# Performance work log

Hardware: AMD Instinct MI355X
Metric: run time of the kernel (lower is better)

Reference implementation:

```python
import jax, jax.numpy as jnp
import numpy as np
import math

CHANNELS = 512
OUT_CHANNELS = 512
N_HEADS = 8
WINDOW = 4
K_CH = CHANNELS // N_HEADS


def _conv1x1(x, W, b):
    # x: (B, C_in, T), W: (C_out, C_in), b: (C_out,)
    return jnp.einsum('oc,bct->bot', W, x) + b[None, :, None]


def _get_relative_embeddings(emb, length, window=WINDOW):
    # emb: (H, 2*window+1, k_ch) -> (H, 2*length-1, k_ch)
    pad_length = max(length - (window + 1), 0)
    start = max(window + 1 - length, 0)
    e = jnp.pad(emb, ((0, 0), (pad_length, pad_length), (0, 0))) if pad_length > 0 else emb
    return e[:, start:start + 2 * length - 1]


def _relative_to_absolute(x):
    # x: (B, H, L, 2L-1) -> (B, H, L, L)
    b, h, L, _ = x.shape
    x = jnp.pad(x, ((0, 0), (0, 0), (0, 0), (0, 1)))          # (B,H,L,2L)
    xf = x.reshape(b, h, L * 2 * L)
    xf = jnp.pad(xf, ((0, 0), (0, 0), (L - 1, 0)))
    return xf.reshape(b, h, L + 1, 2 * L - 1)[:, :, :L, L - 1:]


def _absolute_to_relative(x):
    # x: (B, H, L, L) -> (B, H, L, 2L-1)
    b, h, L, _ = x.shape
    x = jnp.pad(x, ((0, 0), (0, 0), (0, 0), (0, L - 1)))       # (B,H,L,2L-1)
    xf = x.reshape(b, h, L * (2 * L - 1))
    xf = jnp.pad(xf, ((0, 0), (0, 0), (L, 0)))
    return xf.reshape(b, h, L, 2 * L)[:, :, :, 1:]


def setup_inputs() -> dict:
    key = jax.random.key(0)
    ks = jax.random.split(key, 16)
    B, C, T = 4, CHANNELS, 1024
    xavier = math.sqrt(2.0 / (C + C))
    rel_std = K_CH ** -0.5
    return {
        'x_q': jax.random.normal(ks[0], (B, C, T), jnp.float32),
        'x_k': jax.random.normal(ks[1], (B, C, T), jnp.float32),
        'x_v': jax.random.normal(ks[2], (B, C, T), jnp.float32),
        'Wq': jax.random.normal(ks[3], (C, C), jnp.float32) * xavier,
        'bq': jnp.zeros((C,), jnp.float32),
        'Wk': jax.random.normal(ks[4], (C, C), jnp.float32) * xavier,
        'bk': jnp.zeros((C,), jnp.float32),
        'Wv': jax.random.normal(ks[5], (C, C), jnp.float32) * xavier,
        'bv': jnp.zeros((C,), jnp.float32),
        'Wo': jax.random.normal(ks[6], (OUT_CHANNELS, C), jnp.float32) * xavier,
        'bo': jnp.zeros((OUT_CHANNELS,), jnp.float32),
        'emb_rel_k': jax.random.normal(ks[7], (N_HEADS, 2 * WINDOW + 1, K_CH), jnp.float32) * rel_std,
        'emb_rel_v': jax.random.normal(ks[8], (N_HEADS, 2 * WINDOW + 1, K_CH), jnp.float32) * rel_std,
    }


def reference(x_q, x_k, x_v, Wq, bq, Wk, bk, Wv, bv, Wo, bo, emb_rel_k, emb_rel_v):
    q = _conv1x1(x_q, Wq, bq)
    k = _conv1x1(x_k, Wk, bk)
    v = _conv1x1(x_v, Wv, bv)
    B, C, T = q.shape
    # (B, C, T) -> (B, H, T, k_ch); head h owns contiguous k_ch channel chunk
    qh = q.reshape(B, N_HEADS, K_CH, T).transpose(0, 1, 3, 2) / math.sqrt(K_CH)
    kh = k.reshape(B, N_HEADS, K_CH, T).transpose(0, 1, 3, 2)
    vh = v.reshape(B, N_HEADS, K_CH, T).transpose(0, 1, 3, 2)
    scores = jnp.einsum('bhtd,bhsd->bhts', qh, kh)              # (B,H,T,T)
    rel_k = _get_relative_embeddings(emb_rel_k, T)              # (H,2T-1,d)
    rel_logits = jnp.einsum('bhtd,hmd->bhtm', qh, rel_k)        # (B,H,T,2T-1)
    scores = scores + _relative_to_absolute(rel_logits)
    attn = jax.nn.softmax(scores, axis=-1)
    ctx = jnp.einsum('bhts,bhsd->bhtd', attn, vh)
    rel_w = _absolute_to_relative(attn)                         # (B,H,T,2T-1)
    rel_v = _get_relative_embeddings(emb_rel_v, T)
    ctx = ctx + jnp.einsum('bhtm,hmd->bhtd', rel_w, rel_v)
    out = ctx.transpose(0, 1, 3, 2).reshape(B, C, T)
    return _conv1x1(out, Wo, bo)
```

## Files before the change

### kernel.cpp

```cpp
#include <hip/hip_runtime.h>

#define T_LEN 1024
#define NH 8
#define DH 64
#define CCH 512
#define LOG2E 1.44269504088896340736f

typedef _Float16 f16;
typedef _Float16 f16x8 __attribute__((ext_vector_type(8)));
typedef _Float16 f16x4 __attribute__((ext_vector_type(4)));
typedef float f32x4 __attribute__((ext_vector_type(4)));

__device__ __forceinline__ void dma16(const void* g, void* l)
{
    __builtin_amdgcn_global_load_lds((const __attribute__((address_space(1))) void*)g,
                                     (__attribute__((address_space(3))) void*)l, 16, 0, 0);
}

__global__ __launch_bounds__(256)
void prep_kernel(const float* __restrict__ x0, const float* __restrict__ x1,
                 const float* __restrict__ x2, const float* __restrict__ W0,
                 const float* __restrict__ W1, const float* __restrict__ W2,
                 const float* __restrict__ W3, f16* __restrict__ o0,
                 f16* __restrict__ o1, f16* __restrict__ o2, f16* __restrict__ w0,
                 f16* __restrict__ w1, f16* __restrict__ w2, f16* __restrict__ w3,
                 int B)
{
    const int z = blockIdx.z;
    if (z < 3 * B) {
        const int t0 = blockIdx.x * 64, c0 = blockIdx.y * 64;
        const int which = z / B, b = z % B;
        const float* x = (which == 0) ? x0 : (which == 1) ? x1 : x2;
        f16* o = (which == 0) ? o0 : (which == 1) ? o1 : o2;

        __shared__ float L[64 * 68];
        const int cl = threadIdx.x & 63, g = threadIdx.x >> 6;
        const float* src = x + ((size_t)(b * CCH + c0 + cl)) * T_LEN + t0 + g * 16;
        #pragma unroll
        for (int j = 0; j < 4; ++j)
            *(float4*)&L[cl * 68 + g * 16 + 4 * j] = *(const float4*)&src[4 * j];
        __syncthreads();
        const int tl = threadIdx.x & 63, cg = (threadIdx.x >> 6) * 16;
        f16 h[16];
        #pragma unroll
        for (int j = 0; j < 16; ++j) h[j] = (f16)L[(cg + j) * 68 + tl];
        f16* dst = o + ((size_t)(b * T_LEN + t0 + tl)) * CCH + c0 + cg;
        *(f16x8*)&dst[0] = *(f16x8*)&h[0];
        *(f16x8*)&dst[8] = *(f16x8*)&h[8];
    } else {
        const int slice = z - 3 * B;
        size_t i = ((size_t)(slice * 128 + blockIdx.y * 16 + blockIdx.x) * 256 + threadIdx.x) * 4;
        const int wi = (int)(i >> 18);
        const size_t off = i & 262143;
        const float* src = (wi == 0) ? W0 : (wi == 1) ? W1 : (wi == 2) ? W2 : W3;
        f16* dst = (wi == 0) ? w0 : (wi == 1) ? w1 : (wi == 2) ? w2 : w3;
        float4 v4 = *(const float4*)&src[off];
        f16x4 h = {(f16)v4.x, (f16)v4.y, (f16)v4.z, (f16)v4.w};
        *(f16x4*)&dst[off] = h;
    }
}

__global__ __launch_bounds__(256)
void proj_qkv(const f16* __restrict__ xq, const f16* __restrict__ xk,
              const f16* __restrict__ xv, const f16* __restrict__ wq,
              const f16* __restrict__ wk, const f16* __restrict__ wv,
              const float* __restrict__ bq, const float* __restrict__ bk,
              const float* __restrict__ bv, f16* __restrict__ qo,
              f16* __restrict__ ko, f16* __restrict__ vo)
{
    const int which = blockIdx.z;
    const f16* X = (which == 0) ? xq : (which == 1) ? xk : xv;
    const f16* W = (which == 0) ? wq : (which == 1) ? wk : wv;
    const float* bias = (which == 0) ? bq : (which == 1) ? bk : bv;
    const float scale = (which == 0) ? 0.125f * LOG2E : 1.0f;

    const int r0 = blockIdx.x * 64;
    const int o0 = blockIdx.y * 128;
    const int tid = threadIdx.x;
    const int w = tid >> 6, lane = tid & 63;
    const int quad = lane >> 4, l15 = lane & 15;

    __shared__ __align__(16) f16 Xs[64 * 64];
    __shared__ __align__(16) f16 Wsh[128 * 64];

    const int srow = tid >> 3;
    const int scol = ((tid & 7) ^ (srow & 7)) << 3;

    const f16* Xg = X + (size_t)(r0 + srow) * CCH + scol;
    const f16* Wg = W + (size_t)(o0 + srow) * CCH + scol;

    const int ax = (which < 2) ? (w >> 1) : (w & 1);
    const int aw = (which < 2) ? (w & 1) : (w >> 1);

    f32x4 acc[8] = {};

    for (int kc = 0; kc < 8; ++kc) {
        if (kc) __syncthreads();
        const int c1 = kc * 64;
        #pragma unroll
        for (int jj = 0; jj < 4; ++jj)
            dma16(Wg + c1 + (size_t)(32 * jj) * CCH, &Wsh[((size_t)tid + 256 * jj) * 8]);
        #pragma unroll
        for (int jj = 0; jj < 2; ++jj)
            dma16(Xg + c1 + (size_t)(32 * jj) * CCH, &Xs[((size_t)tid + 256 * jj) * 8]);
        __syncthreads();

        #pragma unroll
        for (int ks = 0; ks < 2; ++ks) {
            const int sl = ((ks * 4 + quad) ^ (l15 & 7)) << 3;
            f16x8 xf[2], wf[4];
            #pragma unroll
            for (int i = 0; i < 2; ++i)
                xf[i] = *(const f16x8*)&Xs[(32 * ax + 16 * i + l15) * 64 + sl];
            #pragma unroll
            for (int j = 0; j < 4; ++j)
                wf[j] = *(const f16x8*)&Wsh[(64 * aw + 16 * j + l15) * 64 + sl];
            if (which < 2) {
                #pragma unroll
                for (int i = 0; i < 2; ++i)
                    #pragma unroll
                    for (int j = 0; j < 4; ++j)
                        acc[i * 4 + j] = __builtin_amdgcn_mfma_f32_16x16x32_f16(
                            xf[i], wf[j], acc[i * 4 + j], 0, 0, 0);
            } else {
                #pragma unroll
                for (int i = 0; i < 4; ++i)
                    #pragma unroll
                    for (int j = 0; j < 2; ++j)
                        acc[i * 2 + j] = __builtin_amdgcn_mfma_f32_16x16x32_f16(
                            wf[i], xf[j], acc[i * 2 + j], 0, 0, 0);
            }
        }
    }

    if (which < 2) {
        f16* out = (which == 0) ? qo : ko;
        float bl[4];
        #pragma unroll
        for (int j = 0; j < 4; ++j) bl[j] = bias[o0 + 64 * aw + 16 * j + l15];
        #pragma unroll
        for (int i = 0; i < 2; ++i)
            #pragma unroll
            for (int r = 0; r < 4; ++r) {
                size_t row = (size_t)(r0 + 32 * ax + 16 * i + 4 * quad + r) * CCH;
                #pragma unroll
                for (int j = 0; j < 4; ++j)
                    out[row + o0 + 64 * aw + 16 * j + l15] =
                        (f16)((acc[i * 4 + j][r] + bl[j]) * scale);
            }
    } else {
        const int bb = r0 >> 10, tb = r0 & 1023;
        #pragma unroll
        for (int i = 0; i < 4; ++i) {
            float4 bv4 = *(const float4*)&bias[o0 + 64 * aw + 16 * i + 4 * quad];
            float bl[4] = {bv4.x, bv4.y, bv4.z, bv4.w};
            #pragma unroll
            for (int r = 0; r < 4; ++r) {
                size_t row = ((size_t)(bb * CCH + o0 + 64 * aw + 16 * i + 4 * quad + r)) * T_LEN;
                #pragma unroll
                for (int j = 0; j < 2; ++j)
                    vo[row + tb + 32 * ax + 16 * j + l15] =
                        (f16)(acc[i * 2 + j][r] + bl[r]);
            }
        }
    }
}

__global__ __launch_bounds__(256)
void attn_mfma(const f16* __restrict__ q, const f16* __restrict__ kk,
               const f16* __restrict__ v, const float* __restrict__ ekg,
               const float* __restrict__ evg, f16* __restrict__ ctx)
{
    const int t0 = blockIdx.x * 64, h = blockIdx.y, b = blockIdx.z;
    const int tid = threadIdx.x;
    const int w = tid >> 6, lane = tid & 63;
    const int quad = lane >> 4, l15 = lane & 15;

    __shared__ __align__(16) f16 Qs[4096], Ps[4096];
    __shared__ __align__(16) f16 Ks[2][4096], Vs[2][4096];
    __shared__ float eks[576], evs[576];
    __shared__ float ls[64];

    const int srow = tid >> 3;
    const int scol = ((tid & 7) ^ (srow & 7)) << 3;

    for (int i = tid; i < 576; i += 256) {
        eks[i] = ekg[h * 576 + i];
        evs[i] = evg[h * 576 + i];
    }

    const f16* gk = kk + ((size_t)(b * T_LEN + srow)) * CCH + h * DH + scol;
    const f16* gv = v + ((size_t)(b * CCH + h * DH + srow)) * T_LEN + scol;

    dma16(q + ((size_t)(b * T_LEN + t0 + srow)) * CCH + h * DH + scol, &Qs[(size_t)tid * 8]);
    dma16(q + ((size_t)(b * T_LEN + t0 + srow + 32)) * CCH + h * DH + scol, &Qs[((size_t)tid + 256) * 8]);
    dma16(gk, &Ks[0][(size_t)tid * 8]);
    dma16(gk + (size_t)32 * CCH, &Ks[0][((size_t)tid + 256) * 8]);
    dma16(gv, &Vs[0][(size_t)tid * 8]);
    dma16(gv + (size_t)32 * T_LEN, &Vs[0][((size_t)tid + 256) * 8]);
    __syncthreads();

    f16x8 qf[2];
    #pragma unroll
    for (int ks = 0; ks < 2; ++ks)
        qf[ks] = *(const f16x8*)&Qs[(16 * w + l15) * 64 + (((ks * 4 + quad) ^ (l15 & 7)) << 3)];

    const int myt = 16 * w + l15;
    float Ssum = 0.f;
    f32x4 O[4] = {};

    const bool corner_hi = (blockIdx.x == 0);
    const bool corner_lo = (blockIdx.x == 15);

    for (int it = 0; it < 16; ++it) {
        const int kb = it, cb = it & 1;
        if (it) __syncthreads();

        if (it < 15) {
            const int nb = cb ^ 1;
            dma16(gk + (size_t)((it + 1) * 64) * CCH, &Ks[nb][(size_t)tid * 8]);
            dma16(gk + (size_t)((it + 1) * 64 + 32) * CCH, &Ks[nb][((size_t)tid + 256) * 8]);
            dma16(gv + (it + 1) * 64, &Vs[nb][(size_t)tid * 8]);
            dma16(gv + (size_t)32 * T_LEN + (it + 1) * 64, &Vs[nb][((size_t)tid + 256) * 8]);
        }

        f32x4 S[4] = {};
        #pragma unroll
        for (int ks = 0; ks < 2; ++ks) {
            #pragma unroll
            for (int ct = 0; ct < 4; ++ct) {
                f16x8 aa = *(const f16x8*)&Ks[cb][(16 * ct + l15) * 64 + (((ks * 4 + quad) ^ (l15 & 7)) << 3)];
                S[ct] = __builtin_amdgcn_mfma_f32_16x16x32_f16(aa, qf[ks], S[ct], 0, 0, 0);
            }
        }

        if ((corner_hi && kb == 15) || (corner_lo && kb == 0)) {
            const int s0g = kb * 64;
            #pragma unroll
            for (int ct = 0; ct < 4; ++ct)
                #pragma unroll
                for (int r = 0; r < 4; ++r) {
                    int t_g = t0 + myt;
                    int s_g = s0g + 16 * ct + 4 * quad + r;
                    int df = s_g - t_g;
                    if (df >= 1019 && df <= 1023) {
                        const float* ekp = &eks[(df - 1019) * 64];
                        float sacc = 0.f;
                        for (int d = 0; d < 64; ++d)
                            sacc += (float)Qs[myt * 64 + (((d >> 3) ^ (myt & 7)) << 3) + (d & 7)] * ekp[d];
                        S[ct][r] += sacc;
                    } else if (df >= -1023 && df <= -1021) {
                        const float* ekp = &eks[(1029 + df) * 64];
                        const int t2 = myt - 1;
                        float sacc = 0.f;
                        for (int d = 0; d < 64; ++d)
                            sacc += (float)Qs[t2 * 64 + (((d >> 3) ^ (t2 & 7)) << 3) + (d & 7)] * ekp[d];
                        S[ct][r] += sacc;
                    }
                }
        }

        #pragma unroll
        for (int ct = 0; ct < 4; ++ct) {
            f16x4 pk_;
            #pragma unroll
            for (int r = 0; r < 4; ++r) {
                float p = exp2f(S[ct][r]);
                Ssum += p;
                pk_[r] = (f16)p;
            }
            int colh = (((2 * ct + (quad >> 1)) ^ (myt & 7)) << 3) + (quad & 1) * 4;
            *(f16x4*)&Ps[myt * 64 + colh] = pk_;
        }

        #pragma unroll
        for (int ks = 0; ks < 2; ++ks) {
            f16x8 aa = *(const f16x8*)&Ps[(16 * w + l15) * 64 + (((ks * 4 + quad) ^ (l15 & 7)) << 3)];
            #pragma unroll
            for (int ct = 0; ct < 4; ++ct) {
                f16x8 bf = *(const f16x8*)&Vs[cb][(16 * ct + l15) * 64 + (((ks * 4 + quad) ^ (l15 & 7)) << 3)];
                O[ct] = __builtin_amdgcn_mfma_f32_16x16x32_f16(aa, bf, O[ct], 0, 0, 0);
            }
        }

        const int s0g = kb * 64;
        if (s0g <= t0 + 67 && s0g + 63 >= t0 - 4) {
            #pragma unroll
            for (int r = 0; r < 4; ++r) {
                int t_loc = 16 * w + 4 * quad + r;
                int t_g = t0 + t_loc;
                int slo = max(s0g, t_g - 4), shi = min(s0g + 63, t_g + 4);
                for (int s = slo; s <= shi; ++s) {
                    int sl = s - s0g;
                    float p = (float)Ps[t_loc * 64 + (((sl >> 3) ^ (t_loc & 7)) << 3) + (sl & 7)];
                    const float* evp = &evs[(s - t_g + 4) * 64];
                    #pragma unroll
                    for (int ct = 0; ct < 4; ++ct)
                        O[ct][r] += p * evp[16 * ct + l15];
                }
            }
        }
    }

    Ssum += __shfl_xor(Ssum, 16);
    Ssum += __shfl_xor(Ssum, 32);
    if (quad == 0) ls[myt] = 1.0f / Ssum;
    __syncthreads();

    #pragma unroll
    for (int r = 0; r < 4; ++r) {
        const int t_loc = 16 * w + 4 * quad + r;
        const float rl = ls[t_loc];
        size_t rowo = ((size_t)(b * T_LEN + t0 + t_loc)) * CCH + h * DH;
        #pragma unroll
        for (int ct = 0; ct < 4; ++ct)
            ctx[rowo + 16 * ct + l15] = (f16)(O[ct][r] * rl);
    }
}

__global__ __launch_bounds__(256)
void proj_out(const f16* __restrict__ ctx, const f16* __restrict__ Wo,
              const float* __restrict__ bo, float* __restrict__ out)
{
    const int r0 = blockIdx.x * 64;
    const int o0 = blockIdx.y * 64;
    const int tid = threadIdx.x;
    const int w = tid >> 6, lane = tid & 63;
    const int quad = lane >> 4, l15 = lane & 15;
    const int a  = w >> 1;
    const int b2 = w & 1;

    __shared__ __align__(16) f16 Cs[64 * 64];
    __shared__ __align__(16) f16 Wsh[64 * 64];

    const int srow = tid >> 3;
    const int scol = ((tid & 7) ^ (srow & 7)) << 3;

    const f16* Cg = ctx + (size_t)(r0 + srow) * CCH + scol;
    const f16* Wg = Wo + (size_t)(o0 + srow) * CCH + scol;

    f32x4 acc[2][2] = {};

    for (int kc = 0; kc < 8; ++kc) {
        if (kc) __syncthreads();
        const int c1 = kc * 64;
        #pragma unroll
        for (int jj = 0; jj < 2; ++jj) {
            dma16(Wg + c1 + (size_t)(32 * jj) * CCH, &Wsh[((size_t)tid + 256 * jj) * 8]);
            dma16(Cg + c1 + (size_t)(32 * jj) * CCH, &Cs[((size_t)tid + 256 * jj) * 8]);
        }
        __syncthreads();

        #pragma unroll
        for (int ks = 0; ks < 2; ++ks) {
            const int sl = ((ks * 4 + quad) ^ (l15 & 7)) << 3;
            f16x8 wf[2], cf[2];
            #pragma unroll
            for (int i = 0; i < 2; ++i)
                wf[i] = *(const f16x8*)&Wsh[(32 * a + 16 * i + l15) * 64 + sl];
            #pragma unroll
            for (int j = 0; j < 2; ++j)
                cf[j] = *(const f16x8*)&Cs[(32 * b2 + 16 * j + l15) * 64 + sl];
            #pragma unroll
            for (int i = 0; i < 2; ++i)
                #pragma unroll
                for (int j = 0; j < 2; ++j)
                    acc[i][j] = __builtin_amdgcn_mfma_f32_16x16x32_f16(
                        wf[i], cf[j], acc[i][j], 0, 0, 0);
        }
    }

    const int bb = r0 >> 10, tb = r0 & 1023;
    #pragma unroll
    for (int i = 0; i < 2; ++i) {
        float4 bv4 = *(const float4*)&bo[o0 + 32 * a + 16 * i + 4 * quad];
        float bl[4] = {bv4.x, bv4.y, bv4.z, bv4.w};
        #pragma unroll
        for (int r = 0; r < 4; ++r) {
            size_t row = ((size_t)(bb * CCH + o0 + 32 * a + 16 * i + 4 * quad + r)) * T_LEN;
            #pragma unroll
            for (int j = 0; j < 2; ++j)
                out[row + tb + 32 * b2 + 16 * j + l15] = acc[i][j][r] + bl[r];
        }
    }
}

extern "C" void kernel_launch(void* const* d_in, const int* in_sizes, int n_in,
                              void* d_out, int out_size, void* d_ws, size_t ws_size,
                              hipStream_t stream)
{
    const float* x_q = (const float*)d_in[0];
    const float* x_k = (const float*)d_in[1];
    const float* x_v = (const float*)d_in[2];
    const float* Wq  = (const float*)d_in[3];
    const float* bq  = (const float*)d_in[4];
    const float* Wk  = (const float*)d_in[5];
    const float* bk  = (const float*)d_in[6];
    const float* Wv  = (const float*)d_in[7];
    const float* bv  = (const float*)d_in[8];
    const float* Wo  = (const float*)d_in[9];
    const float* bo  = (const float*)d_in[10];
    const float* erk = (const float*)d_in[11];
    const float* erv = (const float*)d_in[12];

    const int B = in_sizes[0] / (CCH * T_LEN);
    const size_t te = (size_t)B * CCH * T_LEN;
    const size_t we = (size_t)CCH * CCH;

    f16* p = (f16*)d_ws;
    f16* xTq = p; p += te;
    f16* xTk = p; p += te;
    f16* xTv = p; p += te;
    f16* wqh = p; p += we;
    f16* wkh = p; p += we;
    f16* wvh = p; p += we;
    f16* woh = p; p += we;
    f16* qh  = p; p += te;
    f16* kh  = p; p += te;
    f16* vh  = p; p += te;
    f16* ch  = p; p += te;

    dim3 blk(256);
    prep_kernel<<<dim3(16, 8, 3 * B + 8), blk, 0, stream>>>(
        x_q, x_k, x_v, Wq, Wk, Wv, Wo, xTq, xTk, xTv, wqh, wkh, wvh, woh, B);
    proj_qkv<<<dim3(B * 16, 4, 3), blk, 0, stream>>>(
        xTq, xTk, xTv, wqh, wkh, wvh, bq, bk, bv, qh, kh, vh);
    attn_mfma<<<dim3(T_LEN / 64, NH, B), blk, 0, stream>>>(
        qh, kh, vh, erk, erv, ch);
    proj_out<<<dim3(B * 16, 8), blk, 0, stream>>>(
        ch, woh, bo, (float*)d_out);
}
```

Before: 148.5 us.

## Split attention key block across two wave groups with 512-thread blocks

Doubles the attention block to 512 threads. Each group of four waves takes half of each 64-key tile for QK^T and half of the reduction dimension for PV. Each thread now issues a single 16-byte DMA per K/V tile, and the two partial O accumulators and row sums are reduced through shared memory at the end. s_setprio is also raised around the MFMA sections. This is meant to raise wave-level parallelism for a grid of only 512 blocks, at the cost of an extra shared-memory reduction and barrier.

```diff
diff --git a/kernel.cpp b/kernel.cpp
--- a/kernel.cpp
+++ b/kernel.cpp
@@ -166,7 +166,7 @@
     }
 }
 
-__global__ __launch_bounds__(256)
+__global__ __launch_bounds__(512, 4)
 void attn_mfma(const f16* __restrict__ q, const f16* __restrict__ kk,
                const f16* __restrict__ v, const float* __restrict__ ekg,
                const float* __restrict__ evg, f16* __restrict__ ctx)
@@ -175,16 +175,17 @@
     const int tid = threadIdx.x;
     const int w = tid >> 6, lane = tid & 63;
     const int quad = lane >> 4, l15 = lane & 15;
+    const int qw = w & 3, sw = w >> 2;
 
     __shared__ __align__(16) f16 Qs[4096], Ps[4096];
-    __shared__ __align__(16) f16 Ks[2][4096], Vs[2][4096];
+    __shared__ __align__(16) f16 KV[2][2][4096];
     __shared__ float eks[576], evs[576];
-    __shared__ float ls[64];
+    __shared__ float lsp[2][64];
 
     const int srow = tid >> 3;
     const int scol = ((tid & 7) ^ (srow & 7)) << 3;
 
-    for (int i = tid; i < 576; i += 256) {
+    for (int i = tid; i < 576; i += 512) {
         eks[i] = ekg[h * 576 + i];
         evs[i] = evg[h * 576 + i];
     }
@@ -193,19 +194,16 @@
     const f16* gv = v + ((size_t)(b * CCH + h * DH + srow)) * T_LEN + scol;
 
     dma16(q + ((size_t)(b * T_LEN + t0 + srow)) * CCH + h * DH + scol, &Qs[(size_t)tid * 8]);
-    dma16(q + ((size_t)(b * T_LEN + t0 + srow + 32)) * CCH + h * DH + scol, &Qs[((size_t)tid + 256) * 8]);
-    dma16(gk, &Ks[0][(size_t)tid * 8]);
-    dma16(gk + (size_t)32 * CCH, &Ks[0][((size_t)tid + 256) * 8]);
-    dma16(gv, &Vs[0][(size_t)tid * 8]);
-    dma16(gv + (size_t)32 * T_LEN, &Vs[0][((size_t)tid + 256) * 8]);
+    dma16(gk, &KV[0][0][(size_t)tid * 8]);
+    dma16(gv, &KV[0][1][(size_t)tid * 8]);
     __syncthreads();
 
     f16x8 qf[2];
     #pragma unroll
     for (int ks = 0; ks < 2; ++ks)
-        qf[ks] = *(const f16x8*)&Qs[(16 * w + l15) * 64 + (((ks * 4 + quad) ^ (l15 & 7)) << 3)];
-
-    const int myt = 16 * w + l15;
+        qf[ks] = *(const f16x8*)&Qs[(16 * qw + l15) * 64 + (((ks * 4 + quad) ^ (l15 & 7)) << 3)];
+
+    const int myt = 16 * qw + l15;
     float Ssum = 0.f;
     f32x4 O[4] = {};
 
@@ -218,26 +216,29 @@
 
         if (it < 15) {
             const int nb = cb ^ 1;
-            dma16(gk + (size_t)((it + 1) * 64) * CCH, &Ks[nb][(size_t)tid * 8]);
-            dma16(gk + (size_t)((it + 1) * 64 + 32) * CCH, &Ks[nb][((size_t)tid + 256) * 8]);
-            dma16(gv + (it + 1) * 64, &Vs[nb][(size_t)tid * 8]);
-            dma16(gv + (size_t)32 * T_LEN + (it + 1) * 64, &Vs[nb][((size_t)tid + 256) * 8]);
-        }
-
-        f32x4 S[4] = {};
+            dma16(gk + (size_t)((it + 1) * 64) * CCH, &KV[nb][0][(size_t)tid * 8]);
+            dma16(gv + (it + 1) * 64, &KV[nb][1][(size_t)tid * 8]);
+        }
+
+        f32x4 S[2] = {};
+        __builtin_amdgcn_s_setprio(1);
         #pragma unroll
         for (int ks = 0; ks < 2; ++ks) {
             #pragma unroll
-            for (int ct = 0; ct < 4; ++ct) {
-                f16x8 aa = *(const f16x8*)&Ks[cb][(16 * ct + l15) * 64 + (((ks * 4 + quad) ^ (l15 & 7)) << 3)];
-                S[ct] = __builtin_amdgcn_mfma_f32_16x16x32_f16(aa, qf[ks], S[ct], 0, 0, 0);
-            }
-        }
+            for (int cti = 0; cti < 2; ++cti) {
+                const int ct = 2 * sw + cti;
+                f16x8 aa = *(const f16x8*)&KV[cb][0][(16 * ct + l15) * 64 +
+                                                     (((ks * 4 + quad) ^ (l15 & 7)) << 3)];
+                S[cti] = __builtin_amdgcn_mfma_f32_16x16x32_f16(aa, qf[ks], S[cti], 0, 0, 0);
+            }
+        }
+        __builtin_amdgcn_s_setprio(0);
 
         if ((corner_hi && kb == 15) || (corner_lo && kb == 0)) {
             const int s0g = kb * 64;
             #pragma unroll
-            for (int ct = 0; ct < 4; ++ct)
+            for (int cti = 0; cti < 2; ++cti) {
+                const int ct = 2 * sw + cti;
                 #pragma unroll
                 for (int r = 0; r < 4; ++r) {
                     int t_g = t0 + myt;
@@ -248,24 +249,26 @@
                         float sacc = 0.f;
                         for (int d = 0; d < 64; ++d)
                             sacc += (float)Qs[myt * 64 + (((d >> 3) ^ (myt & 7)) << 3) + (d & 7)] * ekp[d];
-                        S[ct][r] += sacc;
+                        S[cti][r] += sacc;
                     } else if (df >= -1023 && df <= -1021) {
                         const float* ekp = &eks[(1029 + df) * 64];
                         const int t2 = myt - 1;
                         float sacc = 0.f;
                         for (int d = 0; d < 64; ++d)
                             sacc += (float)Qs[t2 * 64 + (((d >> 3) ^ (t2 & 7)) << 3) + (d & 7)] * ekp[d];
-                        S[ct][r] += sacc;
+                        S[cti][r] += sacc;
                     }
                 }
-        }
-
-        #pragma unroll
-        for (int ct = 0; ct < 4; ++ct) {
+            }
+        }
+
+        #pragma unroll
+        for (int cti = 0; cti < 2; ++cti) {
+            const int ct = 2 * sw + cti;
             f16x4 pk_;
             #pragma unroll
             for (int r = 0; r < 4; ++r) {
-                float p = exp2f(S[ct][r]);
+                float p = exp2f(S[cti][r]);
                 Ssum += p;
                 pk_[r] = (f16)p;
             }
@@ -273,23 +276,27 @@
             *(f16x4*)&Ps[myt * 64 + colh] = pk_;
         }
 
-        #pragma unroll
-        for (int ks = 0; ks < 2; ++ks) {
-            f16x8 aa = *(const f16x8*)&Ps[(16 * w + l15) * 64 + (((ks * 4 + quad) ^ (l15 & 7)) << 3)];
+        __builtin_amdgcn_s_setprio(1);
+        {
+            f16x8 aa = *(const f16x8*)&Ps[(16 * qw + l15) * 64 +
+                                          (((sw * 4 + quad) ^ (l15 & 7)) << 3)];
             #pragma unroll
             for (int ct = 0; ct < 4; ++ct) {
-                f16x8 bf = *(const f16x8*)&Vs[cb][(16 * ct + l15) * 64 + (((ks * 4 + quad) ^ (l15 & 7)) << 3)];
+                f16x8 bf = *(const f16x8*)&KV[cb][1][(16 * ct + l15) * 64 +
+                                                     (((sw * 4 + quad) ^ (l15 & 7)) << 3)];
                 O[ct] = __builtin_amdgcn_mfma_f32_16x16x32_f16(aa, bf, O[ct], 0, 0, 0);
             }
         }
+        __builtin_amdgcn_s_setprio(0);
 
         const int s0g = kb * 64;
         if (s0g <= t0 + 67 && s0g + 63 >= t0 - 4) {
             #pragma unroll
             for (int r = 0; r < 4; ++r) {
-                int t_loc = 16 * w + 4 * quad + r;
+                int t_loc = 16 * qw + 4 * quad + r;
                 int t_g = t0 + t_loc;
-                int slo = max(s0g, t_g - 4), shi = min(s0g + 63, t_g + 4);
+                int slo = max(max(s0g, t_g - 4), s0g + 32 * sw);
+                int shi = min(min(s0g + 63, t_g + 4), s0g + 32 * sw + 31);
                 for (int s = slo; s <= shi; ++s) {
                     int sl = s - s0g;
                     float p = (float)Ps[t_loc * 64 + (((sl >> 3) ^ (t_loc & 7)) << 3) + (sl & 7)];
@@ -304,17 +311,32 @@
 
     Ssum += __shfl_xor(Ssum, 16);
     Ssum += __shfl_xor(Ssum, 32);
-    if (quad == 0) ls[myt] = 1.0f / Ssum;
+    if (quad == 0) lsp[sw][myt] = Ssum;
     __syncthreads();
 
-    #pragma unroll
-    for (int r = 0; r < 4; ++r) {
-        const int t_loc = 16 * w + 4 * quad + r;
-        const float rl = ls[t_loc];
-        size_t rowo = ((size_t)(b * T_LEN + t0 + t_loc)) * CCH + h * DH;
-        #pragma unroll
-        for (int ct = 0; ct < 4; ++ct)
-            ctx[rowo + 16 * ct + l15] = (f16)(O[ct][r] * rl);
+    float* Ored = (float*)&KV[0][0][0];
+    if (sw == 1) {
+        #pragma unroll
+        for (int r = 0; r < 4; ++r) {
+            const int t_loc = 16 * qw + 4 * quad + r;
+            #pragma unroll
+            for (int ct = 0; ct < 4; ++ct)
+                Ored[t_loc * 66 + 16 * ct + l15] = O[ct][r];
+        }
+    }
+    __syncthreads();
+
+    if (sw == 0) {
+        #pragma unroll
+        for (int r = 0; r < 4; ++r) {
+            const int t_loc = 16 * qw + 4 * quad + r;
+            const float rl = 1.0f / (lsp[0][t_loc] + lsp[1][t_loc]);
+            size_t rowo = ((size_t)(b * T_LEN + t0 + t_loc)) * CCH + h * DH;
+            #pragma unroll
+            for (int ct = 0; ct < 4; ++ct)
+                ctx[rowo + 16 * ct + l15] =
+                    (f16)((O[ct][r] + Ored[t_loc * 66 + 16 * ct + l15]) * rl);
+        }
     }
 }
 
@@ -425,7 +447,7 @@
         x_q, x_k, x_v, Wq, Wk, Wv, Wo, xTq, xTk, xTv, wqh, wkh, wvh, woh, B);
     proj_qkv<<<dim3(B * 16, 4, 3), blk, 0, stream>>>(
         xTq, xTk, xTv, wqh, wkh, wvh, bq, bk, bv, qh, kh, vh);
-    attn_mfma<<<dim3(T_LEN / 64, NH, B), blk, 0, stream>>>(
+    attn_mfma<<<dim3(T_LEN / 64, NH, B), dim3(512), 0, stream>>>(
         qh, kh, vh, erk, erv, ch);
     proj_out<<<dim3(B * 16, 8), blk, 0, stream>>>(
         ch, woh, bo, (float*)d_out);
```

Result: faster. 145.6 us (-2.0%).
